# Optimization experiments

Measured on AMD Instinct MI355X. Metric: run time of the kernel, lower is better.

## Reference

```python
import jax, jax.numpy as jnp
import numpy as np

B, N, E, DIN = 2048, 38, 4, 9
H0, H1, L0 = 256, 256, 512
EPS = 1e-5
_mask_np = np.ones((N, DIN), np.float32)
_mask_np[np.arange(0, N, 2), :] = 0.0
MASK = jnp.asarray(_mask_np)  # (N, DIN); masked rows zeroed


def _bn_relu(h, g, b):
    # h: (B, N, 1, D); BatchNorm2d(N) normalizes over (batch, H=1, W=D) per node channel
    mu = jnp.mean(h, axis=(0, 2, 3), keepdims=True)
    var = jnp.var(h, axis=(0, 2, 3), keepdims=True)  # biased var, as torch BN
    h = (h - mu) * jax.lax.rsqrt(var + EPS) * g[None, :, None, None] + b[None, :, None, None]
    return jax.nn.relu(h)


def _gconv(adj, nodes, Ws, bs, We, be):
    # adj: (B, E, N, N); nodes: (B, N, 1, Din)
    out = Ws.shape[0]
    hs = nodes @ Ws.T + bs  # self term: (B, N, 1, out)
    m = (nodes @ We.T + be).reshape(nodes.shape[0], N, out, E)
    hr = jnp.einsum('bemn,bnce->bmc', adj, m)  # relational aggregation
    return hs + hr[:, :, None, :]


def _forward(adj, x, cWs0, cbs0, cWe0, cbe0, cg0, cb0, cWs1, cbs1, cWe1, cbe1, cg1, cb1, lW0, lb0, lg0, lbb0, fW, fb):
    masked_x = MASK * x
    h = masked_x[:, :, None, :]
    h = _bn_relu(_gconv(adj, h, cWs0, cbs0, cWe0, cbe0), cg0, cb0)
    h = _bn_relu(_gconv(adj, h, cWs1, cbs1, cWe1, cbe1), cg1, cb1)
    h = _bn_relu(h @ lW0.T + lb0, lg0, lbb0)
    h = (h @ fW.T + fb)[:, :, 0, :]  # (B, N, 2*DIN)
    s_logits, t = h[..., :DIN], h[..., DIN:]
    s = jax.nn.sigmoid(s_logits)
    out = masked_x + (1.0 - MASK) * (x + t) * s
    logdet = jnp.sum(jax.nn.log_sigmoid(s_logits).reshape(x.shape[0], -1), axis=1)
    return out, logdet


def setup_inputs() -> dict:
    key = jax.random.key(0)
    ks = jax.random.split(key, 8)
    rn = lambda k, shape: jax.random.normal(ks[k], shape, jnp.float32) * 0.1
    return {
        'adj': jax.random.uniform(ks[0], (B, E, N, N), jnp.float32),
        'x': jax.random.normal(ks[1], (B, N, DIN), jnp.float32),
        'cWs0': rn(2, (H0, DIN)), 'cbs0': jnp.zeros((H0,), jnp.float32),
        'cWe0': rn(3, (H0 * E, DIN)), 'cbe0': jnp.zeros((H0 * E,), jnp.float32),
        'cg0': jnp.ones((N,), jnp.float32), 'cb0': jnp.zeros((N,), jnp.float32),
        'cWs1': rn(4, (H1, H0)), 'cbs1': jnp.zeros((H1,), jnp.float32),
        'cWe1': rn(5, (H1 * E, H0)), 'cbe1': jnp.zeros((H1 * E,), jnp.float32),
        'cg1': jnp.ones((N,), jnp.float32), 'cb1': jnp.zeros((N,), jnp.float32),
        'lW0': rn(6, (L0, H1)), 'lb0': jnp.zeros((L0,), jnp.float32),
        'lg0': jnp.ones((N,), jnp.float32), 'lbb0': jnp.zeros((N,), jnp.float32),
        'fW': rn(7, (2 * DIN, L0)), 'fb': jnp.zeros((2 * DIN,), jnp.float32),
    }


def reference(adj, x, cWs0, cbs0, cWe0, cbe0, cg0, cb0, cWs1, cbs1, cWe1, cbe1, cg1, cb1, lW0, lb0, lg0, lbb0, fW, fb):
    return _forward(adj, x, cWs0, cbs0, cWe0, cbe0, cg0, cb0, cWs1, cbs1, cWe1, cbe1, cg1, cb1, lW0, lb0, lg0, lbb0, fW, fb)
```

## Files before the change

kernel.cpp:

```cpp
#include <hip/hip_runtime.h>
#include <hip/hip_bf16.h>
#include <math.h>

#define B_   2048
#define N_   38
#define E_   4
#define DIN_ 9
#define H0_  256
#define H1_  256
#define L0_  512
#define M_   (B_ * N_)

typedef short bf16x8 __attribute__((ext_vector_type(8)));
typedef float f32x4 __attribute__((ext_vector_type(4)));

__device__ __forceinline__ float b2f(unsigned short u) {
  return __uint_as_float((unsigned)u << 16);
}
__device__ __forceinline__ unsigned short f2b(float f) {
  __hip_bfloat16 h = __float2bfloat16(f);
  return *(unsigned short*)&h;
}

__device__ __forceinline__ float rsum16(float v) {
  v += __shfl_xor(v, 1);
  v += __shfl_xor(v, 2);
  v += __shfl_xor(v, 4);
  v += __shfl_xor(v, 8);
  return v;
}

__global__ void k_build_wg0(const float* __restrict__ Ws, const float* __restrict__ bs,
                            const float* __restrict__ We, const float* __restrict__ be,
                            unsigned short* __restrict__ WT) {
  int i = blockIdx.x * 256 + threadIdx.x;
  if (i >= 256 * 96) return;
  int c = i / 96, k = i % 96;
  float v = 0.f;
  if (k < 64) {
    int e = k >> 4, f = k & 15;
    if (f < 9) v = We[(c * 4 + e) * 9 + f];
    else if (f == 9) v = be[c * 4 + e];
  } else if (k < 80) {
    int f = k - 64;
    if (f < 9) v = Ws[c * 9 + f];
    else if (f == 9) v = bs[c];
  }
  WT[i] = f2b(v);
}

__global__ void k_build_wcat(const float* __restrict__ Ws, const float* __restrict__ We,
                             unsigned short* __restrict__ WT) {
  int i = blockIdx.x * 256 + threadIdx.x;
  if (i >= 256 * 1280) return;
  int c = i / 1280, k = i % 1280;
  float v;
  if (k < 256) v = Ws[c * 256 + k];
  else { int kk = k - 256; int e = kk >> 8, f = kk & 255; v = We[(c * 4 + e) * 256 + f]; }
  WT[i] = f2b(v);
}

__global__ void k_build_wl(const float* __restrict__ W, unsigned short* __restrict__ WT) {
  int i = blockIdx.x * 256 + threadIdx.x;
  if (i >= 512 * 256) return;
  WT[i] = f2b(W[i]);
}

__global__ void k_build_wf(const float* __restrict__ W, unsigned short* __restrict__ WT) {
  int i = blockIdx.x * 256 + threadIdx.x;
  if (i >= 32 * 512) return;
  int r = i / 512, k = i % 512;
  WT[i] = f2b(r < 18 ? W[r * 512 + k] : 0.f);
}

__global__ __launch_bounds__(256) void k_gred(const float* __restrict__ part, int nblk,
                                              float* __restrict__ st) {
  const int j = blockIdx.x, tid = threadIdx.x;
  float s = 0.f;
  for (int i = tid; i < nblk; i += 256) s += part[(size_t)i * 76 + j];
#pragma unroll
  for (int off = 32; off; off >>= 1) s += __shfl_down(s, off);
  __shared__ float r[4];
  if ((tid & 63) == 0) r[tid >> 6] = s;
  __syncthreads();
  if (tid == 0) {
    float tot = r[0] + r[1] + r[2] + r[3];
    if (j < 38) st[j * 2] = tot;
    else st[(j - 38) * 2 + 1] = tot;
  }
}

__global__ __launch_bounds__(256) void k_gconv0(
    const float* __restrict__ adj, const float* __restrict__ x,
    const unsigned short* __restrict__ Wg0, unsigned short* __restrict__ g,
    float* __restrict__ part) {
  __shared__ __align__(16) unsigned short adjB[4 * 48 * 64];
  __shared__ __align__(16) unsigned short zB[48 * 64];
  __shared__ __align__(16) unsigned short xLA[64 * 32];
  __shared__ __align__(16) unsigned short xLB[16 * 64];
  __shared__ float lsumW[4][48], lsqW[4][48];
  const int b = blockIdx.x, t = threadIdx.x;
  const uint4 z4 = make_uint4(0, 0, 0, 0);
  for (int i = t; i < 4 * 48 * 64 / 8; i += 256) ((uint4*)adjB)[i] = z4;
  for (int i = t; i < 64 * 32 / 8; i += 256) ((uint4*)xLA)[i] = z4;
  for (int i = t; i < 16 * 64 / 8; i += 256) ((uint4*)xLB)[i] = z4;
  __syncthreads();
  for (int i = t; i < 4 * 38 * 38; i += 256) {
    int e = i / 1444, r = i % 1444, m = r / 38, n = r % 38;
    adjB[(e * 48 + m) * 64 + n] = f2b(adj[(size_t)b * 5776 + i]);
  }
  for (int i = t; i < 342; i += 256) {
    int m = i / 9, f = i % 9;
    float v = x[(size_t)b * 342 + i];
    unsigned short bv = f2b((m & 1) ? v : 0.f);
    xLA[m * 32 + f] = bv;
    xLB[f * 64 + m] = bv;
  }
  if (t < 38) {
    unsigned short one = f2b(1.f);
    xLA[t * 32 + 9] = one;
    xLB[9 * 64 + t] = one;
  }
  __syncthreads();
  const int w = t >> 6, L = t & 63;
  const int lrow = L & 15, quad = L >> 4;
  {
    f32x4 za[3];
#pragma unroll
    for (int mt = 0; mt < 3; ++mt) za[mt] = (f32x4){0.f, 0.f, 0.f, 0.f};
#pragma unroll
    for (int kk = 0; kk < 2; ++kk) {
      bf16x8 bb = *(const bf16x8*)&xLB[lrow * 64 + kk * 32 + quad * 8];
#pragma unroll
      for (int mt = 0; mt < 3; ++mt) {
        bf16x8 aa = *(const bf16x8*)&adjB[(w * 48 + mt * 16 + lrow) * 64 + kk * 32 + quad * 8];
        za[mt] = __builtin_amdgcn_mfma_f32_16x16x32_bf16(aa, bb, za[mt], 0, 0, 0);
      }
    }
#pragma unroll
    for (int mt = 0; mt < 3; ++mt)
#pragma unroll
      for (int reg = 0; reg < 4; ++reg)
        zB[(mt * 16 + quad * 4 + reg) * 64 + w * 16 + lrow] = f2b(za[mt][reg]);
  }
  __syncthreads();
  f32x4 acc[3][4];
#pragma unroll
  for (int mt = 0; mt < 3; ++mt)
#pragma unroll
    for (int nt = 0; nt < 4; ++nt) acc[mt][nt] = (f32x4){0.f, 0.f, 0.f, 0.f};
#pragma unroll
  for (int kc = 0; kc < 3; ++kc) {
    bf16x8 af[3];
#pragma unroll
    for (int mt = 0; mt < 3; ++mt)
      af[mt] = (kc < 2)
                   ? *(const bf16x8*)&zB[(mt * 16 + lrow) * 64 + kc * 32 + quad * 8]
                   : *(const bf16x8*)&xLA[(mt * 16 + lrow) * 32 + quad * 8];
#pragma unroll
    for (int nt = 0; nt < 4; ++nt) {
      const int c = w * 64 + nt * 16 + lrow;
      bf16x8 bf_ = *(const bf16x8*)&Wg0[(size_t)c * 96 + kc * 32 + quad * 8];
#pragma unroll
      for (int mt = 0; mt < 3; ++mt)
        acc[mt][nt] = __builtin_amdgcn_mfma_f32_16x16x32_bf16(af[mt], bf_, acc[mt][nt], 0, 0, 0);
    }
  }
#pragma unroll
  for (int mt = 0; mt < 3; ++mt) {
#pragma unroll
    for (int reg = 0; reg < 4; ++reg) {
      const int m = mt * 16 + quad * 4 + reg;
      float sv = 0.f, qv = 0.f;
      if (m < N_) {
#pragma unroll
        for (int nt = 0; nt < 4; ++nt) {
          const int c = w * 64 + nt * 16 + lrow;
          float v = acc[mt][nt][reg];
          g[((size_t)b * N_ + m) * 256 + c] = f2b(v);
          sv += v;
          qv += v * v;
        }
      }
      sv = rsum16(sv);
      qv = rsum16(qv);
      if (lrow == 0) { lsumW[w][m] = sv; lsqW[w][m] = qv; }
    }
  }
  __syncthreads();
  if (t < 38) {
    part[(size_t)b * 76 + t] = lsumW[0][t] + lsumW[1][t] + lsumW[2][t] + lsumW[3][t];
    part[(size_t)b * 76 + 38 + t] = lsqW[0][t] + lsqW[1][t] + lsqW[2][t] + lsqW[3][t];
  }
}

__global__ __launch_bounds__(256, 2) void k_l1f(
    const float* __restrict__ adj, const unsigned short* __restrict__ g0,
    const unsigned short* __restrict__ Wcat, const float* __restrict__ st0,
    const float* __restrict__ gam, const float* __restrict__ bet,
    const float* __restrict__ bs, const float* __restrict__ be,
    unsigned short* __restrict__ h2, float* __restrict__ part) {
  __shared__ __align__(16) unsigned short Pbuf[48 * 256];
  __shared__ __align__(16) unsigned short adjC[4 * 40 * 40];
  __shared__ float aS[38], bS[38];
  __shared__ float arowS[4 * 38];
  __shared__ float lsumW[4][48], lsqW[4][48];
  const int b = blockIdx.x, t = threadIdx.x;
  for (int i = t; i < 800; i += 256) ((uint4*)adjC)[i] = make_uint4(0, 0, 0, 0);
  if (t < 38) {
    const float cnt = 2048.f * 256.f;
    float mu = st0[t * 2] / cnt;
    float var = st0[t * 2 + 1] / cnt - mu * mu;
    float a = rsqrtf(var + 1e-5f) * gam[t];
    aS[t] = a;
    bS[t] = bet[t] - mu * a;
  }
  __syncthreads();
  for (int i = t; i < 4 * 38 * 19; i += 256) {
    int e = i / 722, r = i % 722, m = r / 19, p2 = r % 19;
    float2 v = *(const float2*)&adj[(size_t)b * 5776 + e * 1444 + m * 38 + 2 * p2];
    unsigned pk = (unsigned)f2b(v.x) | ((unsigned)f2b(v.y) << 16);
    *(unsigned*)&adjC[(e * 40 + m) * 40 + 2 * p2] = pk;
  }
  for (int i = t; i < 38 * 32; i += 256) {
    int n = i >> 5, seg = (i & 31) * 8;
    uint4 u = *(const uint4*)&g0[((size_t)b * N_ + n) * 256 + seg];
    float a = aS[n], bb2 = bS[n];
    unsigned* up = (unsigned*)&u;
    uint4 o;
    unsigned* op = (unsigned*)&o;
#pragma unroll
    for (int j = 0; j < 4; ++j) {
      float lo = fmaxf(fmaf(b2f((unsigned short)(up[j] & 0xffff)), a, bb2), 0.f);
      float hi = fmaxf(fmaf(b2f((unsigned short)(up[j] >> 16)), a, bb2), 0.f);
      op[j] = (unsigned)f2b(lo) | ((unsigned)f2b(hi) << 16);
    }
    *(uint4*)((char*)Pbuf + n * 512 + ((seg * 2) ^ ((n & 7) << 4))) = o;
  }
  for (int i = t; i < 10 * 32; i += 256) {
    int n = 38 + (i >> 5), seg = (i & 31) * 8;
    *(uint4*)((char*)Pbuf + n * 512 + ((seg * 2) ^ ((n & 7) << 4))) = make_uint4(0, 0, 0, 0);
  }
  __syncthreads();
  const int w = t >> 6, L = t & 63;
  const int lrow = L & 15, quad = L >> 4;
  const int swzL = (lrow & 7) << 4;
  bf16x8 bbr[2][4];
#pragma unroll
  for (int kk = 0; kk < 2; ++kk)
#pragma unroll
    for (int nt = 0; nt < 4; ++nt) {
      const int c2 = 2 * (w * 64 + nt * 16 + lrow);
      unsigned pk[4];
#pragma unroll
      for (int jp = 0; jp < 4; ++jp) {
        int n0 = kk * 32 + quad * 8 + 2 * jp;
        int na = n0 < 48 ? n0 : 47;
        int nb = (n0 + 1) < 48 ? (n0 + 1) : 47;
        unsigned short lo =
            *(const unsigned short*)((const char*)Pbuf + na * 512 + (c2 ^ ((na & 7) << 4)));
        unsigned short hi =
            *(const unsigned short*)((const char*)Pbuf + nb * 512 + (c2 ^ ((nb & 7) << 4)));
        pk[jp] = (unsigned)lo | ((unsigned)hi << 16);
      }
      union { unsigned u[4]; bf16x8 v; } uu;
      uu.u[0] = pk[0]; uu.u[1] = pk[1]; uu.u[2] = pk[2]; uu.u[3] = pk[3];
      bbr[kk][nt] = uu.v;
    }
  if (t < 152) {
    int e2 = t / 38, m2 = t % 38;
    float s = 0.f;
    for (int n = 0; n < 38; ++n) s += b2f(adjC[(e2 * 40 + m2) * 40 + n]);
    arowS[e2 * 38 + m2] = s;
  }

  f32x4 acc[3][4];
#pragma unroll
  for (int mt = 0; mt < 3; ++mt)
#pragma unroll
    for (int nt = 0; nt < 4; ++nt) acc[mt][nt] = (f32x4){0.f, 0.f, 0.f, 0.f};

#define MAIN_KBLOCK(WOFF)                                                              \
  _Pragma("unroll") for (int kc = 0; kc < 8; ++kc) {                                   \
    bf16x8 af[3];                                                                      \
    _Pragma("unroll") for (int mt = 0; mt < 3; ++mt) af[mt] =                          \
        *(const bf16x8*)((const char*)Pbuf + (mt * 16 + lrow) * 512 +                  \
                         ((kc * 64 + quad * 16) ^ swzL));                              \
    _Pragma("unroll") for (int nt = 0; nt < 4; ++nt) {                                 \
      const int c = w * 64 + nt * 16 + lrow;                                           \
      bf16x8 bf_ = *(const bf16x8*)&Wcat[(size_t)c * 1280 + (WOFF) + kc * 32 + quad * 8]; \
      _Pragma("unroll") for (int mt = 0; mt < 3; ++mt) acc[mt][nt] =                   \
          __builtin_amdgcn_mfma_f32_16x16x32_bf16(af[mt], bf_, acc[mt][nt], 0, 0, 0);  \
    }                                                                                  \
  }

#define PCOMPUTE(H, PA)                                                                \
  do {                                                                                 \
    _Pragma("unroll") for (int mt = 0; mt < 3; ++mt)                                   \
        _Pragma("unroll") for (int q2 = 0; q2 < 2; ++q2)                               \
            PA[mt][q2] = (f32x4){0.f, 0.f, 0.f, 0.f};                                  \
    _Pragma("unroll") for (int kk = 0; kk < 2; ++kk) {                                 \
      _Pragma("unroll") for (int mt = 0; mt < 3; ++mt) {                               \
        const int ma = mt * 16 + lrow;                                                 \
        const int mr = ma < 40 ? ma : 0;                                               \
        const int cb = (kk == 0) ? (quad * 8) : (quad == 0 ? 32 : 0);                  \
        bf16x8 aa = *(const bf16x8*)&adjC[(e * 40 + mr) * 40 + cb];                    \
        const bool okf = (ma < 40) && (kk == 0 || quad == 0);                          \
        if (!okf) aa = (bf16x8){0, 0, 0, 0, 0, 0, 0, 0};                               \
        PA[mt][0] = __builtin_amdgcn_mfma_f32_16x16x32_bf16(aa, bbr[kk][(H)*2 + 0],    \
                                                            PA[mt][0], 0, 0, 0);       \
        PA[mt][1] = __builtin_amdgcn_mfma_f32_16x16x32_bf16(aa, bbr[kk][(H)*2 + 1],    \
                                                            PA[mt][1], 0, 0, 0);       \
      }                                                                                \
    }                                                                                  \
  } while (0)

#define PSTORE(H, PA)                                                                  \
  do {                                                                                 \
    _Pragma("unroll") for (int mt = 0; mt < 3; ++mt)                                   \
        _Pragma("unroll") for (int reg = 0; reg < 4; ++reg) {                          \
      const int m = mt * 16 + quad * 4 + reg;                                          \
      _Pragma("unroll") for (int q2 = 0; q2 < 2; ++q2) {                               \
        const int c2 = w * 64 + ((H)*2 + q2) * 16 + lrow;                              \
        *(unsigned short*)((char*)Pbuf + m * 512 + ((2 * c2) ^ ((m & 7) << 4))) =      \
            f2b(PA[mt][q2][reg]);                                                      \
      }                                                                                \
    }                                                                                  \
  } while (0)

  MAIN_KBLOCK(0)

#pragma unroll 1
  for (int e = 0; e < 4; ++e) {
    f32x4 pa[3][2];
    PCOMPUTE(0, pa);
    __syncthreads();
    PSTORE(0, pa);
    PCOMPUTE(1, pa);
    PSTORE(1, pa);
    __syncthreads();
    MAIN_KBLOCK(256 + e * 256)
  }
#undef PSTORE
#undef PCOMPUTE
#undef MAIN_KBLOCK

#pragma unroll
  for (int mt = 0; mt < 3; ++mt) {
#pragma unroll
    for (int reg = 0; reg < 4; ++reg) {
      const int m = mt * 16 + quad * 4 + reg;
      float sv = 0.f, qv = 0.f;
      if (m < N_) {
        float a0 = arowS[0 * 38 + m], a1 = arowS[38 + m];
        float a2 = arowS[76 + m], a3 = arowS[114 + m];
#pragma unroll
        for (int nt = 0; nt < 4; ++nt) {
          const int col = w * 64 + nt * 16 + lrow;
          float4 bev = *(const float4*)&be[col * 4];
          float v = acc[mt][nt][reg] + bs[col] +
                    a0 * bev.x + a1 * bev.y + a2 * bev.z + a3 * bev.w;
          h2[((size_t)b * N_ + m) * 256 + col] = f2b(v);
          sv += v;
          qv += v * v;
        }
      }
      sv = rsum16(sv);
      qv = rsum16(qv);
      if (lrow == 0) { lsumW[w][m] = sv; lsqW[w][m] = qv; }
    }
  }
  __syncthreads();
  if (t < 38) {
    part[(size_t)b * 76 + t] = lsumW[0][t] + lsumW[1][t] + lsumW[2][t] + lsumW[3][t];
    part[(size_t)b * 76 + 38 + t] = lsqW[0][t] + lsqW[1][t] + lsqW[2][t] + lsqW[3][t];
  }
}

template <bool BIAS, bool STATS>
__global__ __launch_bounds__(512) void k_gemm(
    const unsigned short* __restrict__ A0, const unsigned short* __restrict__ Bw,
    const float* __restrict__ bias, const float* __restrict__ stIn,
    const float* __restrict__ gam, const float* __restrict__ bet, float cnt,
    unsigned short* __restrict__ Cout, int Cstride, float* __restrict__ part) {
  __shared__ __align__(16) unsigned short lA[128 * 32];
  __shared__ __align__(16) unsigned short lB[256 * 32];
  __shared__ float lbias[256];
  __shared__ float lsum[38], lsq[38];
  const int t = threadIdx.x;
  const int tileM = blockIdx.x, n_base = blockIdx.y * 256;
  if (BIAS && t < 256) lbias[t] = bias[n_base + t];
  if (STATS && t < 38) { lsum[t] = 0.f; lsq[t] = 0.f; }
  const int w = t >> 6, L = t & 63;
  const int wr = w >> 2, wc = w & 3;
  const int lrow = L & 15, quad = L >> 4;
  const int srow = t >> 2, sseg = (t & 3) * 8;
  const int nA = (tileM * 128 + srow) % 38;
  float aC, bC;
  {
    float mu = stIn[nA * 2] / cnt;
    float var = stIn[nA * 2 + 1] / cnt - mu * mu;
    aC = rsqrtf(var + 1e-5f) * gam[nA];
    bC = bet[nA] - mu * aC;
  }
  const unsigned short* aRow = A0 + (size_t)(tileM * 128 + srow) * 256 + sseg;
  f32x4 acc[4][4];
#pragma unroll
  for (int mt = 0; mt < 4; ++mt)
#pragma unroll
    for (int nt = 0; nt < 4; ++nt) acc[mt][nt] = (f32x4){0.f, 0.f, 0.f, 0.f};

  uint4 u = *(const uint4*)aRow;
  for (int ki = 0; ki < 8; ++ki) {
#pragma unroll
    for (int r = 0; r < 2; ++r) {
      const unsigned short* gp = Bw + (size_t)(n_base + r * 128 + srow) * 256 + ki * 32 + sseg;
      __builtin_amdgcn_global_load_lds(
          (const __attribute__((address_space(1))) void*)gp,
          (__attribute__((address_space(3))) void*)(lB + r * 4096 + w * 512), 16, 0, 0);
    }
    uint4 un = u;
    if (ki < 7) un = *(const uint4*)(aRow + (ki + 1) * 32);
    {
      uint4 o;
      unsigned* up = (unsigned*)&u;
      unsigned* op = (unsigned*)&o;
#pragma unroll
      for (int j = 0; j < 4; ++j) {
        float lo = fmaxf(fmaf(b2f((unsigned short)(up[j] & 0xffff)), aC, bC), 0.f);
        float hi = fmaxf(fmaf(b2f((unsigned short)(up[j] >> 16)), aC, bC), 0.f);
        op[j] = (unsigned)f2b(lo) | ((unsigned)f2b(hi) << 16);
      }
      *(uint4*)&lA[srow * 32 + sseg] = o;
    }
    __syncthreads();
    bf16x8 af[4], bfr[4];
#pragma unroll
    for (int mt = 0; mt < 4; ++mt)
      af[mt] = *(const bf16x8*)&lA[(wr * 64 + mt * 16 + lrow) * 32 + quad * 8];
#pragma unroll
    for (int nt = 0; nt < 4; ++nt)
      bfr[nt] = *(const bf16x8*)&lB[(wc * 64 + nt * 16 + lrow) * 32 + quad * 8];
#pragma unroll
    for (int mt = 0; mt < 4; ++mt)
#pragma unroll
      for (int nt = 0; nt < 4; ++nt)
        acc[mt][nt] = __builtin_amdgcn_mfma_f32_16x16x32_bf16(af[mt], bfr[nt], acc[mt][nt], 0, 0, 0);
    __syncthreads();
    u = un;
  }
#pragma unroll
  for (int mt = 0; mt < 4; ++mt) {
#pragma unroll
    for (int reg = 0; reg < 4; ++reg) {
      const size_t row = (size_t)tileM * 128 + wr * 64 + mt * 16 + quad * 4 + reg;
      float sv = 0.f, qv = 0.f;
#pragma unroll
      for (int nt = 0; nt < 4; ++nt) {
        const int lcol = wc * 64 + nt * 16 + lrow;
        float v = acc[mt][nt][reg];
        if (BIAS) v += lbias[lcol];
        Cout[row * Cstride + n_base + lcol] = f2b(v);
        sv += v;
        qv += v * v;
      }
      if (STATS) {
        sv = rsum16(sv);
        qv = rsum16(qv);
        if (lrow == 0) {
          int n = (int)(row % 38);
          atomicAdd(&lsum[n], sv);
          atomicAdd(&lsq[n], qv);
        }
      }
    }
  }
  if (STATS) {
    __syncthreads();
    const int blk = blockIdx.y * gridDim.x + blockIdx.x;
    if (t < 38) {
      part[(size_t)blk * 76 + t] = lsum[t];
      part[(size_t)blk * 76 + 38 + t] = lsq[t];
    }
  }
}

__global__ __launch_bounds__(256) void k_final(
    const unsigned short* __restrict__ g2, const float* __restrict__ x,
    const unsigned short* __restrict__ Wfb, const float* __restrict__ fb,
    const float* __restrict__ st, const float* __restrict__ gam,
    const float* __restrict__ bet, float* __restrict__ out) {
  __shared__ __align__(16) unsigned short hA[48 * 520];
  __shared__ float lgS[48 * 20];
  __shared__ float aS[N_], bS[N_], fbS[20], red[4];
  const int b = blockIdx.x, tid = threadIdx.x;
  if (tid < N_) {
    const float cnt = 2048.f * 512.f;
    float mu = st[tid * 2] / cnt;
    float var = st[tid * 2 + 1] / cnt - mu * mu;
    float a = rsqrtf(var + 1e-5f) * gam[tid];
    aS[tid] = a;
    bS[tid] = bet[tid] - mu * a;
  }
  if (tid >= 64 && tid < 82) fbS[tid - 64] = fb[tid - 64];
  __syncthreads();
  for (int i = tid; i < N_ * 64; i += 256) {
    int n = i >> 6, seg = (i & 63) * 8;
    uint4 u = *(const uint4*)&g2[((size_t)b * N_ + n) * 512 + seg];
    float a = aS[n], bb = bS[n];
    float v[8];
    v[0] = b2f((unsigned short)(u.x & 0xffff)); v[1] = b2f((unsigned short)(u.x >> 16));
    v[2] = b2f((unsigned short)(u.y & 0xffff)); v[3] = b2f((unsigned short)(u.y >> 16));
    v[4] = b2f((unsigned short)(u.z & 0xffff)); v[5] = b2f((unsigned short)(u.z >> 16));
    v[6] = b2f((unsigned short)(u.w & 0xffff)); v[7] = b2f((unsigned short)(u.w >> 16));
#pragma unroll
    for (int j = 0; j < 8; ++j) v[j] = fmaxf(fmaf(v[j], a, bb), 0.f);
    uint4 o;
    o.x = (unsigned)f2b(v[0]) | ((unsigned)f2b(v[1]) << 16);
    o.y = (unsigned)f2b(v[2]) | ((unsigned)f2b(v[3]) << 16);
    o.z = (unsigned)f2b(v[4]) | ((unsigned)f2b(v[5]) << 16);
    o.w = (unsigned)f2b(v[6]) | ((unsigned)f2b(v[7]) << 16);
    *(uint4*)&hA[n * 520 + seg] = o;
  }
  for (int i = tid; i < 10 * 64; i += 256) {
    int n = 38 + (i >> 6), seg = (i & 63) * 8;
    *(uint4*)&hA[n * 520 + seg] = make_uint4(0, 0, 0, 0);
  }
  __syncthreads();
  const int w = tid >> 6, L = tid & 63;
  const int lrow = L & 15, quad = L >> 4;
  if (w < 3) {
    f32x4 acc0 = (f32x4){0.f, 0.f, 0.f, 0.f}, acc1 = (f32x4){0.f, 0.f, 0.f, 0.f};
#pragma unroll
    for (int ki = 0; ki < 16; ++ki) {
      bf16x8 af = *(const bf16x8*)&hA[(w * 16 + lrow) * 520 + ki * 32 + quad * 8];
      bf16x8 b0 = *(const bf16x8*)&Wfb[(size_t)lrow * 512 + ki * 32 + quad * 8];
      bf16x8 b1 = *(const bf16x8*)&Wfb[(size_t)(16 + lrow) * 512 + ki * 32 + quad * 8];
      acc0 = __builtin_amdgcn_mfma_f32_16x16x32_bf16(af, b0, acc0, 0, 0, 0);
      acc1 = __builtin_amdgcn_mfma_f32_16x16x32_bf16(af, b1, acc1, 0, 0, 0);
    }
#pragma unroll
    for (int reg = 0; reg < 4; ++reg) {
      int m = w * 16 + quad * 4 + reg;
      if (m < N_) {
        lgS[m * 20 + lrow] = acc0[reg] + fbS[lrow];
        if (lrow < 2) lgS[m * 20 + 16 + lrow] = acc1[reg] + fbS[16 + lrow];
      }
    }
  }
  __syncthreads();
  float ls = 0.f;
  for (int ii = tid; ii < 342; ii += 256) {
    int mm = ii / 9, d = ii % 9;
    float sl = lgS[mm * 20 + d];
    float tv = lgS[mm * 20 + 9 + d];
    float xv = x[((size_t)b * N_ + mm) * 9 + d];
    float sg = 1.f / (1.f + expf(-sl));
    float o = (mm & 1) ? xv : (xv + tv) * sg;
    out[((size_t)b * N_ + mm) * 9 + d] = o;
    ls += (sl >= 0.f) ? -log1pf(expf(-sl)) : (sl - log1pf(expf(sl)));
  }
#pragma unroll
  for (int off = 32; off; off >>= 1) ls += __shfl_down(ls, off);
  if (L == 0) red[w] = ls;
  __syncthreads();
  if (tid == 0) out[(size_t)B_ * 342 + b] = red[0] + red[1] + red[2] + red[3];
}

extern "C" void kernel_launch(void* const* d_in, const int* in_sizes, int n_in,
                              void* d_out, int out_size, void* d_ws, size_t ws_size,
                              hipStream_t stream) {
  (void)in_sizes; (void)n_in; (void)out_size; (void)ws_size;
  const float* adj  = (const float*)d_in[0];
  const float* x    = (const float*)d_in[1];
  const float* cWs0 = (const float*)d_in[2];
  const float* cbs0 = (const float*)d_in[3];
  const float* cWe0 = (const float*)d_in[4];
  const float* cbe0 = (const float*)d_in[5];
  const float* cg0  = (const float*)d_in[6];
  const float* cb0  = (const float*)d_in[7];
  const float* cWs1 = (const float*)d_in[8];
  const float* cbs1 = (const float*)d_in[9];
  const float* cWe1 = (const float*)d_in[10];
  const float* cbe1 = (const float*)d_in[11];
  const float* cg1  = (const float*)d_in[12];
  const float* cb1  = (const float*)d_in[13];
  const float* lW0  = (const float*)d_in[14];
  const float* lb0  = (const float*)d_in[15];
  const float* lg0  = (const float*)d_in[16];
  const float* lbb0 = (const float*)d_in[17];
  const float* fW   = (const float*)d_in[18];
  const float* fb   = (const float*)d_in[19];
  float* out = (float*)d_out;

  char* p = (char*)d_ws;
  float* stats = (float*)p;                     p += 1024;
  unsigned short* Wg0  = (unsigned short*)p;    p += 256 * 96 * 2;
  unsigned short* Wfb  = (unsigned short*)p;    p += 32 * 512 * 2;
  unsigned short* Wcat = (unsigned short*)p;    p += 256 * 1280 * 2;
  unsigned short* Wl   = (unsigned short*)p;    p += 512 * 256 * 2;
  float* part0 = (float*)p;                     p += 2048 * 76 * 4;
  float* part1 = (float*)p;                     p += 2048 * 76 * 4;
  float* part2 = (float*)p;                     p += 1216 * 76 * 4;
  unsigned short* g0   = (unsigned short*)p;    p += (size_t)M_ * 256 * 2;
  unsigned short* h2   = (unsigned short*)p;    p += (size_t)M_ * 256 * 2;
  unsigned short* g2   = (unsigned short*)p;

  float* st0 = stats;
  float* st1 = stats + 76;
  float* st2 = stats + 152;

  k_build_wg0<<<96, 256, 0, stream>>>(cWs0, cbs0, cWe0, cbe0, Wg0);
  k_build_wcat<<<1280, 256, 0, stream>>>(cWs1, cWe1, Wcat);
  k_build_wl<<<512, 256, 0, stream>>>(lW0, Wl);
  k_build_wf<<<64, 256, 0, stream>>>(fW, Wfb);

  k_gconv0<<<2048, 256, 0, stream>>>(adj, x, Wg0, g0, part0);
  k_gred<<<76, 256, 0, stream>>>(part0, 2048, st0);

  k_l1f<<<2048, 256, 0, stream>>>(adj, g0, Wcat, st0, cg0, cb0, cbs1, cbe1, h2, part1);
  k_gred<<<76, 256, 0, stream>>>(part1, 2048, st1);

  k_gemm<true, true><<<dim3(608, 2), 512, 0, stream>>>(
      h2, Wl, lb0, st1, cg1, cb1, 2048.f * 256.f, g2, 512, part2);
  k_gred<<<76, 256, 0, stream>>>(part2, 1216, st2);

  k_final<<<2048, 256, 0, stream>>>(g2, x, Wfb, fb, st2, lg0, lbb0, out);
}
```

Before: 466.0 us.

## Process two batch graphs per block in fused layer-1 gconv kernel

The fused layer-1 kernel now handles two batch elements per workgroup, doubling the M tiles so each Wcat B-fragment loaded from global memory feeds six MFMAs instead of three. Grid size halves and shared buffers double, with the stats scratch aliased onto the adjacency buffer. This aims to halve weight traffic per output row, at the cost of more registers (acc[6][4], pa[6][2], bbr[2][2][4]) and more LDS, which may lower occupancy under the launch bound of 2.

```diff
diff --git a/kernel.cpp b/kernel.cpp
--- a/kernel.cpp
+++ b/kernel.cpp
@@ -200,13 +200,12 @@
     const float* __restrict__ gam, const float* __restrict__ bet,
     const float* __restrict__ bs, const float* __restrict__ be,
     unsigned short* __restrict__ h2, float* __restrict__ part) {
-  __shared__ __align__(16) unsigned short Pbuf[48 * 256];
-  __shared__ __align__(16) unsigned short adjC[4 * 40 * 40];
+  __shared__ __align__(16) unsigned short Pbuf[2 * 48 * 256];
+  __shared__ __align__(16) unsigned short adjC[2 * 4 * 40 * 40];
   __shared__ float aS[38], bS[38];
-  __shared__ float arowS[4 * 38];
-  __shared__ float lsumW[4][48], lsqW[4][48];
-  const int b = blockIdx.x, t = threadIdx.x;
-  for (int i = t; i < 800; i += 256) ((uint4*)adjC)[i] = make_uint4(0, 0, 0, 0);
+  __shared__ float arowS[2 * 4 * 38];
+  const int b0 = blockIdx.x * 2, t = threadIdx.x;
+  for (int i = t; i < 1600; i += 256) ((uint4*)adjC)[i] = make_uint4(0, 0, 0, 0);
   if (t < 38) {
     const float cnt = 2048.f * 256.f;
     float mu = st0[t * 2] / cnt;
@@ -216,15 +215,17 @@
     bS[t] = bet[t] - mu * a;
   }
   __syncthreads();
-  for (int i = t; i < 4 * 38 * 19; i += 256) {
-    int e = i / 722, r = i % 722, m = r / 19, p2 = r % 19;
-    float2 v = *(const float2*)&adj[(size_t)b * 5776 + e * 1444 + m * 38 + 2 * p2];
+  for (int i = t; i < 2 * 4 * 38 * 19; i += 256) {
+    int bsel = i / 2888, r0 = i % 2888;
+    int e = r0 / 722, r = r0 % 722, m = r / 19, p2 = r % 19;
+    float2 v = *(const float2*)&adj[(size_t)(b0 + bsel) * 5776 + e * 1444 + m * 38 + 2 * p2];
     unsigned pk = (unsigned)f2b(v.x) | ((unsigned)f2b(v.y) << 16);
-    *(unsigned*)&adjC[(e * 40 + m) * 40 + 2 * p2] = pk;
-  }
-  for (int i = t; i < 38 * 32; i += 256) {
-    int n = i >> 5, seg = (i & 31) * 8;
-    uint4 u = *(const uint4*)&g0[((size_t)b * N_ + n) * 256 + seg];
+    *(unsigned*)&adjC[bsel * 6400 + (e * 40 + m) * 40 + 2 * p2] = pk;
+  }
+  for (int i = t; i < 2 * 38 * 32; i += 256) {
+    int bsel = i / 1216, r = i % 1216;
+    int n = r >> 5, seg = (r & 31) * 8;
+    uint4 u = *(const uint4*)&g0[((size_t)(b0 + bsel) * N_ + n) * 256 + seg];
     float a = aS[n], bb2 = bS[n];
     unsigned* up = (unsigned*)&u;
     uint4 o;
@@ -235,81 +236,87 @@
       float hi = fmaxf(fmaf(b2f((unsigned short)(up[j] >> 16)), a, bb2), 0.f);
       op[j] = (unsigned)f2b(lo) | ((unsigned)f2b(hi) << 16);
     }
-    *(uint4*)((char*)Pbuf + n * 512 + ((seg * 2) ^ ((n & 7) << 4))) = o;
-  }
-  for (int i = t; i < 10 * 32; i += 256) {
-    int n = 38 + (i >> 5), seg = (i & 31) * 8;
-    *(uint4*)((char*)Pbuf + n * 512 + ((seg * 2) ^ ((n & 7) << 4))) = make_uint4(0, 0, 0, 0);
+    const int row = bsel * 48 + n;
+    *(uint4*)((char*)Pbuf + row * 512 + ((seg * 2) ^ ((row & 7) << 4))) = o;
+  }
+  for (int i = t; i < 2 * 10 * 32; i += 256) {
+    int bsel = i / 320, r = i % 320;
+    int row = bsel * 48 + 38 + (r >> 5), seg = (r & 31) * 8;
+    *(uint4*)((char*)Pbuf + row * 512 + ((seg * 2) ^ ((row & 7) << 4))) = make_uint4(0, 0, 0, 0);
   }
   __syncthreads();
   const int w = t >> 6, L = t & 63;
   const int lrow = L & 15, quad = L >> 4;
   const int swzL = (lrow & 7) << 4;
-  bf16x8 bbr[2][4];
-#pragma unroll
-  for (int kk = 0; kk < 2; ++kk)
-#pragma unroll
-    for (int nt = 0; nt < 4; ++nt) {
-      const int c2 = 2 * (w * 64 + nt * 16 + lrow);
-      unsigned pk[4];
-#pragma unroll
-      for (int jp = 0; jp < 4; ++jp) {
-        int n0 = kk * 32 + quad * 8 + 2 * jp;
-        int na = n0 < 48 ? n0 : 47;
-        int nb = (n0 + 1) < 48 ? (n0 + 1) : 47;
-        unsigned short lo =
-            *(const unsigned short*)((const char*)Pbuf + na * 512 + (c2 ^ ((na & 7) << 4)));
-        unsigned short hi =
-            *(const unsigned short*)((const char*)Pbuf + nb * 512 + (c2 ^ ((nb & 7) << 4)));
-        pk[jp] = (unsigned)lo | ((unsigned)hi << 16);
-      }
-      union { unsigned u[4]; bf16x8 v; } uu;
-      uu.u[0] = pk[0]; uu.u[1] = pk[1]; uu.u[2] = pk[2]; uu.u[3] = pk[3];
-      bbr[kk][nt] = uu.v;
-    }
-  if (t < 152) {
-    int e2 = t / 38, m2 = t % 38;
+  bf16x8 bbr[2][2][4];
+#pragma unroll
+  for (int bsel = 0; bsel < 2; ++bsel)
+#pragma unroll
+    for (int kk = 0; kk < 2; ++kk)
+#pragma unroll
+      for (int nt = 0; nt < 4; ++nt) {
+        const int c2 = 2 * (w * 64 + nt * 16 + lrow);
+        unsigned pk[4];
+#pragma unroll
+        for (int jp = 0; jp < 4; ++jp) {
+          int n0 = kk * 32 + quad * 8 + 2 * jp;
+          int na = bsel * 48 + (n0 < 48 ? n0 : 47);
+          int nb = bsel * 48 + ((n0 + 1) < 48 ? (n0 + 1) : 47);
+          unsigned short lo =
+              *(const unsigned short*)((const char*)Pbuf + na * 512 + (c2 ^ ((na & 7) << 4)));
+          unsigned short hi =
+              *(const unsigned short*)((const char*)Pbuf + nb * 512 + (c2 ^ ((nb & 7) << 4)));
+          pk[jp] = (unsigned)lo | ((unsigned)hi << 16);
+        }
+        union { unsigned u[4]; bf16x8 v; } uu;
+        uu.u[0] = pk[0]; uu.u[1] = pk[1]; uu.u[2] = pk[2]; uu.u[3] = pk[3];
+        bbr[bsel][kk][nt] = uu.v;
+      }
+  if (t < 304) {
+    int bsel = t / 152, r = t % 152;
+    int e2 = r / 38, m2 = r % 38;
     float s = 0.f;
-    for (int n = 0; n < 38; ++n) s += b2f(adjC[(e2 * 40 + m2) * 40 + n]);
-    arowS[e2 * 38 + m2] = s;
-  }
-
-  f32x4 acc[3][4];
-#pragma unroll
-  for (int mt = 0; mt < 3; ++mt)
+    for (int n = 0; n < 38; ++n) s += b2f(adjC[bsel * 6400 + (e2 * 40 + m2) * 40 + n]);
+    arowS[bsel * 152 + e2 * 38 + m2] = s;
+  }
+
+  f32x4 acc[6][4];
+#pragma unroll
+  for (int mt = 0; mt < 6; ++mt)
 #pragma unroll
     for (int nt = 0; nt < 4; ++nt) acc[mt][nt] = (f32x4){0.f, 0.f, 0.f, 0.f};
 
 #define MAIN_KBLOCK(WOFF)                                                              \
   _Pragma("unroll") for (int kc = 0; kc < 8; ++kc) {                                   \
-    bf16x8 af[3];                                                                      \
-    _Pragma("unroll") for (int mt = 0; mt < 3; ++mt) af[mt] =                          \
+    bf16x8 af[6];                                                                      \
+    _Pragma("unroll") for (int mt = 0; mt < 6; ++mt) af[mt] =                          \
         *(const bf16x8*)((const char*)Pbuf + (mt * 16 + lrow) * 512 +                  \
                          ((kc * 64 + quad * 16) ^ swzL));                              \
     _Pragma("unroll") for (int nt = 0; nt < 4; ++nt) {                                 \
       const int c = w * 64 + nt * 16 + lrow;                                           \
       bf16x8 bf_ = *(const bf16x8*)&Wcat[(size_t)c * 1280 + (WOFF) + kc * 32 + quad * 8]; \
-      _Pragma("unroll") for (int mt = 0; mt < 3; ++mt) acc[mt][nt] =                   \
+      _Pragma("unroll") for (int mt = 0; mt < 6; ++mt) acc[mt][nt] =                   \
           __builtin_amdgcn_mfma_f32_16x16x32_bf16(af[mt], bf_, acc[mt][nt], 0, 0, 0);  \
     }                                                                                  \
   }
 
 #define PCOMPUTE(H, PA)                                                                \
   do {                                                                                 \
-    _Pragma("unroll") for (int mt = 0; mt < 3; ++mt)                                   \
+    _Pragma("unroll") for (int mt = 0; mt < 6; ++mt)                                   \
         _Pragma("unroll") for (int q2 = 0; q2 < 2; ++q2)                               \
             PA[mt][q2] = (f32x4){0.f, 0.f, 0.f, 0.f};                                  \
     _Pragma("unroll") for (int kk = 0; kk < 2; ++kk) {                                 \
-      _Pragma("unroll") for (int mt = 0; mt < 3; ++mt) {                               \
-        const int ma = mt * 16 + lrow;                                                 \
+      _Pragma("unroll") for (int mt = 0; mt < 6; ++mt) {                               \
+        const int bsel = mt / 3, mtl = mt % 3;                                         \
+        const int ma = mtl * 16 + lrow;                                                \
         const int mr = ma < 40 ? ma : 0;                                               \
         const int cb = (kk == 0) ? (quad * 8) : (quad == 0 ? 32 : 0);                  \
-        bf16x8 aa = *(const bf16x8*)&adjC[(e * 40 + mr) * 40 + cb];                    \
+        bf16x8 aa = *(const bf16x8*)&adjC[bsel * 6400 + (e * 40 + mr) * 40 + cb];      \
         const bool okf = (ma < 40) && (kk == 0 || quad == 0);                          \
         if (!okf) aa = (bf16x8){0, 0, 0, 0, 0, 0, 0, 0};                               \
-        PA[mt][0] = __builtin_amdgcn_mfma_f32_16x16x32_bf16(aa, bbr[kk][(H)*2 + 0],    \
+        PA[mt][0] = __builtin_amdgcn_mfma_f32_16x16x32_bf16(aa, bbr[bsel][kk][(H)*2 + 0], \
                                                             PA[mt][0], 0, 0, 0);       \
-        PA[mt][1] = __builtin_amdgcn_mfma_f32_16x16x32_bf16(aa, bbr[kk][(H)*2 + 1],    \
+        PA[mt][1] = __builtin_amdgcn_mfma_f32_16x16x32_bf16(aa, bbr[bsel][kk][(H)*2 + 1], \
                                                             PA[mt][1], 0, 0, 0);       \
       }                                                                                \
     }                                                                                  \
@@ -317,12 +324,14 @@
 
 #define PSTORE(H, PA)                                                                  \
   do {                                                                                 \
-    _Pragma("unroll") for (int mt = 0; mt < 3; ++mt)                                   \
+    _Pragma("unroll") for (int mt = 0; mt < 6; ++mt)                                   \
         _Pragma("unroll") for (int reg = 0; reg < 4; ++reg) {                          \
-      const int m = mt * 16 + quad * 4 + reg;                                          \
+      const int bsel = mt / 3;                                                         \
+      const int m = (mt % 3) * 16 + quad * 4 + reg;                                    \
+      const int row = bsel * 48 + m;                                                   \
       _Pragma("unroll") for (int q2 = 0; q2 < 2; ++q2) {                               \
         const int c2 = w * 64 + ((H)*2 + q2) * 16 + lrow;                              \
-        *(unsigned short*)((char*)Pbuf + m * 512 + ((2 * c2) ^ ((m & 7) << 4))) =      \
+        *(unsigned short*)((char*)Pbuf + row * 512 + ((2 * c2) ^ ((row & 7) << 4))) =  \
             f2b(PA[mt][q2][reg]);                                                      \
       }                                                                                \
     }                                                                                  \
@@ -332,7 +341,7 @@
 
 #pragma unroll 1
   for (int e = 0; e < 4; ++e) {
-    f32x4 pa[3][2];
+    f32x4 pa[6][2];
     PCOMPUTE(0, pa);
     __syncthreads();
     PSTORE(0, pa);
@@ -345,35 +354,46 @@
 #undef PCOMPUTE
 #undef MAIN_KBLOCK
 
-#pragma unroll
-  for (int mt = 0; mt < 3; ++mt) {
+  float* lsumW = (float*)adjC;
+  float* lsqW  = lsumW + 4 * 96;
+#pragma unroll
+  for (int mt = 0; mt < 6; ++mt) {
 #pragma unroll
     for (int reg = 0; reg < 4; ++reg) {
-      const int m = mt * 16 + quad * 4 + reg;
+      const int bsel = mt / 3;
+      const int m = (mt % 3) * 16 + quad * 4 + reg;
       float sv = 0.f, qv = 0.f;
       if (m < N_) {
-        float a0 = arowS[0 * 38 + m], a1 = arowS[38 + m];
-        float a2 = arowS[76 + m], a3 = arowS[114 + m];
+        float a0 = arowS[bsel * 152 + 0 * 38 + m], a1 = arowS[bsel * 152 + 38 + m];
+        float a2 = arowS[bsel * 152 + 76 + m], a3 = arowS[bsel * 152 + 114 + m];
 #pragma unroll
         for (int nt = 0; nt < 4; ++nt) {
           const int col = w * 64 + nt * 16 + lrow;
           float4 bev = *(const float4*)&be[col * 4];
           float v = acc[mt][nt][reg] + bs[col] +
                     a0 * bev.x + a1 * bev.y + a2 * bev.z + a3 * bev.w;
-          h2[((size_t)b * N_ + m) * 256 + col] = f2b(v);
+          h2[((size_t)(b0 + bsel) * N_ + m) * 256 + col] = f2b(v);
           sv += v;
           qv += v * v;
         }
       }
       sv = rsum16(sv);
       qv = rsum16(qv);
-      if (lrow == 0) { lsumW[w][m] = sv; lsqW[w][m] = qv; }
+      if (lrow == 0) { lsumW[w * 96 + bsel * 48 + m] = sv; lsqW[w * 96 + bsel * 48 + m] = qv; }
     }
   }
   __syncthreads();
   if (t < 38) {
-    part[(size_t)b * 76 + t] = lsumW[0][t] + lsumW[1][t] + lsumW[2][t] + lsumW[3][t];
-    part[(size_t)b * 76 + 38 + t] = lsqW[0][t] + lsqW[1][t] + lsqW[2][t] + lsqW[3][t];
+    float s0 = 0.f, q0 = 0.f, s1 = 0.f, q1 = 0.f;
+#pragma unroll
+    for (int ww = 0; ww < 4; ++ww) {
+      s0 += lsumW[ww * 96 + t];       q0 += lsqW[ww * 96 + t];
+      s1 += lsumW[ww * 96 + 48 + t];  q1 += lsqW[ww * 96 + 48 + t];
+    }
+    part[(size_t)b0 * 76 + t] = s0;
+    part[(size_t)b0 * 76 + 38 + t] = q0;
+    part[(size_t)(b0 + 1) * 76 + t] = s1;
+    part[(size_t)(b0 + 1) * 76 + 38 + t] = q1;
   }
 }
 
@@ -618,7 +638,7 @@
   k_gconv0<<<2048, 256, 0, stream>>>(adj, x, Wg0, g0, part0);
   k_gred<<<76, 256, 0, stream>>>(part0, 2048, st0);
 
-  k_l1f<<<2048, 256, 0, stream>>>(adj, g0, Wcat, st0, cg0, cb0, cbs1, cbe1, h2, part1);
+  k_l1f<<<1024, 256, 0, stream>>>(adj, g0, Wcat, st0, cg0, cb0, cbs1, cbe1, h2, part1);
   k_gred<<<76, 256, 0, stream>>>(part1, 2048, st1);
 
   k_gemm<true, true><<<dim3(608, 2), 512, 0, stream>>>(
```

Result: no change. 465.5 us (-0.1%).
